# Optimization experiments

Hardware: AMD Instinct MI355X
Metric: run time of the kernel (lower is better)

The kernel has to match this reference:

```python
import jax, jax.numpy as jnp
import numpy as np
from jax import lax

B, H, W = 16, 256, 256
NUM_HIDDEN = 12
C = 3 + NUM_HIDDEN + 1  # 16 channels: rgb + hidden + alpha
HID = 64
ALPHA = 1.0
THR = 0.1

SOBEL_X = jnp.array([[-1.0, 0.0, 1.0], [-2.0, 0.0, 2.0], [-1.0, 0.0, 1.0]], jnp.float32) / 8.0
SOBEL_Y = jnp.array([[-1.0, -2.0, -1.0], [0.0, 0.0, 0.0], [1.0, 2.0, 1.0]], jnp.float32) / 8.0


def _sobel_conv(s, k):
    # s: [B,H,W] channel-summed state; k: [3,3]. SAME-padded 2D stencil.
    return lax.conv_general_dilated(
        s[..., None], k[:, :, None, None], window_strides=(1, 1), padding='SAME',
        dimension_numbers=('NHWC', 'HWIO', 'NHWC'))  # [B,H,W,1]


def _alive(x, thr):
    # 3x3 max-pool over alpha channel (index 3), SAME padding.
    a = x[..., 3:4]
    pooled = lax.reduce_window(a, -jnp.inf, lax.max, (1, 3, 3, 1), (1, 1, 1, 1), 'SAME')
    return pooled > thr  # [B,H,W,1] bool


def setup_inputs() -> dict:
    key = jax.random.key(0)
    ks = jax.random.split(key, 7)
    x = jax.random.uniform(ks[0], (B, H, W, C), dtype=jnp.float32)
    # UpdateNet params: 1x1 convs stored as dense matrices [in, out].
    w1 = jax.random.normal(ks[1], (3 * C, HID), dtype=jnp.float32) * (1.0 / np.sqrt(3 * C))
    b1 = jnp.zeros((HID,), jnp.float32)
    w2 = jax.random.normal(ks[2], (HID, HID), dtype=jnp.float32) * (1.0 / np.sqrt(HID))
    b2 = jnp.zeros((HID,), jnp.float32)
    # Original zero-inits w3; use small random values so outputs/grads are nontrivial.
    w3 = jax.random.normal(ks[3], (HID, C), dtype=jnp.float32) * 0.01
    return {'x': x, 'w1': w1, 'b1': b1, 'w2': w2, 'b2': b2, 'w3': w3}


def reference(x, w1, b1, w2, b2, w3):
    pre_life = _alive(x, THR)
    # Sobel perception: kernel[o,i] = sobel for all o,i  =>  each output channel
    # is the sobel filter applied to the channel-sum; broadcast across C channels.
    s = jnp.sum(x, axis=-1)                      # [B,H,W]
    sx = _sobel_conv(s, SOBEL_X)                 # [B,H,W,1]
    sy = _sobel_conv(s, SOBEL_Y)                 # [B,H,W,1]
    perc = jnp.concatenate(
        [x, jnp.broadcast_to(sx, x.shape), jnp.broadcast_to(sy, x.shape)], axis=-1)  # [B,H,W,3C]
    # UpdateNet: two biased 1x1 convs + ReLU, then unbiased 1x1 conv.
    h = jax.nn.relu(jnp.einsum('bhwi,io->bhwo', perc, w1) + b1)
    h = jax.nn.relu(jnp.einsum('bhwi,io->bhwo', h, w2) + b2)
    update = jnp.einsum('bhwi,io->bhwo', h, w3)  # [B,H,W,C]
    # cell_fire_rate == 1.0 -> stochastic update mask is all ones.
    x_new = x + ALPHA * update
    post_life = _alive(x_new, THR)
    life = (pre_life & post_life).astype(x_new.dtype)
    return x_new * life
```

## Files before the change

### kernel.cpp

```cpp
#include <hip/hip_runtime.h>
#include <hip/hip_bf16.h>
#include <cstdint>

#define NPIX (16 * 256 * 256)
#define THRV 0.1f

typedef __bf16 bf16x8 __attribute__((ext_vector_type(8)));
typedef float  f32x4  __attribute__((ext_vector_type(4)));

#define NSLOT 18

__global__ __launch_bounds__(64) void k_pack(const float* __restrict__ w1,
                                             const float* __restrict__ b1,
                                             const float* __restrict__ w2,
                                             const float* __restrict__ b2,
                                             const float* __restrict__ w3,
                                             float4* __restrict__ wpack) {
    const int lane = threadIdx.x;
    const int r = lane & 15, g = lane >> 4;
#pragma unroll
    for (int n = 0; n < 4; ++n) {
        const int cc = n * 16 + r;
        bf16x8 f;
#pragma unroll
        for (int j = 0; j < 8; ++j) {
            float v = 0.f;
            if (j < 4) v = w1[(g * 4 + j) * 64 + cc];
            else if (g == 0 && j == 4) { for (int t = 0; t < 16; ++t) v += w1[(16 + t) * 64 + cc]; }
            else if (g == 0 && j == 5) { for (int t = 0; t < 16; ++t) v += w1[(32 + t) * 64 + cc]; }
            else if (g == 1 && j == 4) v = b1[cc];
            f[j] = (__bf16)v;
        }
        wpack[n * 64 + lane] = *(const float4*)&f;
    }
#pragma unroll
    for (int s = 0; s < 2; ++s)
#pragma unroll
        for (int n = 0; n < 4; ++n) {
            bf16x8 f;
#pragma unroll
            for (int j = 0; j < 8; ++j) {
                const int psi = (2 * s + (j >> 2)) * 16 + g * 4 + (j & 3);
                f[j] = (__bf16)w2[psi * 64 + n * 16 + r];
            }
            wpack[(4 + s * 4 + n) * 64 + lane] = *(const float4*)&f;
        }
#pragma unroll
    for (int s = 0; s < 2; ++s) {
        bf16x8 f;
#pragma unroll
        for (int j = 0; j < 8; ++j) {
            const int psi = (2 * s + (j >> 2)) * 16 + g * 4 + (j & 3);
            f[j] = (__bf16)w3[psi * 16 + r];
        }
        wpack[(12 + s) * 64 + lane] = *(const float4*)&f;
    }
#pragma unroll
    for (int n = 0; n < 4; ++n) {
        f32x4 v;
#pragma unroll
        for (int q = 0; q < 4; ++q) v[q] = b2[n * 16 + g * 4 + q];
        wpack[(14 + n) * 64 + lane] = *(const float4*)&v;
    }
}

__global__ __launch_bounds__(256) void k_fused(const float* __restrict__ x,
                                               const float4* __restrict__ wpack,
                                               float* __restrict__ out,
                                               unsigned char* __restrict__ rpre,
                                               unsigned char* __restrict__ anewf) {
    __shared__ float sH0[256], sC[256], sH2[256], sC3[256];

    const int tid = threadIdx.x;
    const int wv = tid >> 6, lane = tid & 63;
    const int r = lane & 15, g = lane >> 4;

    const int row = (blockIdx.x & 7) * 512 + (blockIdx.x >> 3);
    const int y = row & 255;
    const size_t rbase = (size_t)row * 256;
    const int wcol = wv * 64;
    const bool ymok = (y > 0), ypok = (y < 255);

    float4 ha0 = {0,0,0,0}, ha1 = {0,0,0,0}, ha2 = {0,0,0,0}, ha3 = {0,0,0,0};
    float4 hb0 = {0,0,0,0}, hb1 = {0,0,0,0}, hb2 = {0,0,0,0}, hb3 = {0,0,0,0};
    if (ymok) {
        const float4* pm = (const float4*)(x + (rbase - 256 + tid) * 16);
        ha0 = pm[0]; ha1 = pm[1]; ha2 = pm[2]; ha3 = pm[3];
    }
    if (ypok) {
        const float4* pp = (const float4*)(x + (rbase + 256 + tid) * 16);
        hb0 = pp[0]; hb1 = pp[1]; hb2 = pp[2]; hb3 = pp[3];
    }
    float4 xf[4];
#pragma unroll
    for (int t = 0; t < 4; ++t) {
        const int col = wcol + t * 16 + r;
        xf[t] = *(const float4*)(x + (rbase + col) * 16 + g * 4);
    }

    const float s0 = ((ha0.x + ha0.y) + (ha0.z + ha0.w)) + ((ha1.x + ha1.y) + (ha1.z + ha1.w)) +
                     ((ha2.x + ha2.y) + (ha2.z + ha2.w)) + ((ha3.x + ha3.y) + (ha3.z + ha3.w));
    const float s2 = ((hb0.x + hb0.y) + (hb0.z + hb0.w)) + ((hb1.x + hb1.y) + (hb1.z + hb1.w)) +
                     ((hb2.x + hb2.y) + (hb2.z + hb2.w)) + ((hb3.x + hb3.y) + (hb3.z + hb3.w));
    sH0[tid] = s0;
    sH2[tid] = s2;

#pragma unroll
    for (int t = 0; t < 4; ++t) {
        const int col = wcol + t * 16 + r;
        float p = (xf[t].x + xf[t].y) + (xf[t].z + xf[t].w);
        p += __shfl_xor(p, 16);
        p += __shfl_xor(p, 32);
        if (g == 0) { sC[col] = p; sC3[col] = xf[t].w; }
    }
    __syncthreads();

    bf16x8 w1f[4], w2f[2][4], w3f[2];
    f32x4 b2v[4];
#pragma unroll
    for (int n = 0; n < 4; ++n) { float4 t = wpack[n * 64 + lane]; w1f[n] = *(bf16x8*)&t; }
#pragma unroll
    for (int s2i = 0; s2i < 2; ++s2i)
#pragma unroll
        for (int n = 0; n < 4; ++n) { float4 t = wpack[(4 + s2i * 4 + n) * 64 + lane]; w2f[s2i][n] = *(bf16x8*)&t; }
#pragma unroll
    for (int s2i = 0; s2i < 2; ++s2i) { float4 t = wpack[(12 + s2i) * 64 + lane]; w3f[s2i] = *(bf16x8*)&t; }
#pragma unroll
    for (int n = 0; n < 4; ++n) { float4 t = wpack[(14 + n) * 64 + lane]; b2v[n] = *(f32x4*)&t; }

#pragma unroll
    for (int t = 0; t < 4; ++t) {
        const int col = wcol + t * 16 + r;
        const size_t pix = rbase + col;
        const bool cl = (col > 0), cr = (col < 255);

        const float r0m = cl ? sH0[col - 1] : 0.f;
        const float r0c = sH0[col];
        const float r0p = cr ? sH0[col + 1] : 0.f;
        const float r1m = cl ? sC[col - 1] : 0.f;
        const float r1p = cr ? sC[col + 1] : 0.f;
        const float r2m = cl ? sH2[col - 1] : 0.f;
        const float r2c = sH2[col];
        const float r2p = cr ? sH2[col + 1] : 0.f;
        const float gx = ((r0p - r0m) + 2.f * (r1p - r1m) + (r2p - r2m)) * 0.125f;
        const float gy = ((r2m + 2.f * r2c + r2p) - (r0m + 2.f * r0c + r0p)) * 0.125f;

        if (g == 0) {
            const float c3m = cl ? sC3[col - 1] : 0.f;
            const float c3c = sC3[col];
            const float c3p = cr ? sC3[col + 1] : 0.f;
            rpre[pix] = (fmaxf(c3m, fmaxf(c3c, c3p)) > THRV) ? 1 : 0;
        }

        bf16x8 a1;
        a1[0] = (__bf16)xf[t].x; a1[1] = (__bf16)xf[t].y;
        a1[2] = (__bf16)xf[t].z; a1[3] = (__bf16)xf[t].w;
        a1[4] = (__bf16)(g == 0 ? gx : (g == 1 ? 1.f : 0.f));
        a1[5] = (__bf16)(g == 0 ? gy : 0.f);
        a1[6] = (__bf16)0.f; a1[7] = (__bf16)0.f;

        f32x4 acc1[4];
#pragma unroll
        for (int n = 0; n < 4; ++n)
            acc1[n] = __builtin_amdgcn_mfma_f32_16x16x32_bf16(
                w1f[n], a1, (f32x4){0.f, 0.f, 0.f, 0.f}, 0, 0, 0);

        bf16x8 bf2[2];
#pragma unroll
        for (int s2i = 0; s2i < 2; ++s2i)
#pragma unroll
            for (int j = 0; j < 4; ++j) {
                bf2[s2i][j]     = (__bf16)fmaxf(acc1[2 * s2i][j], 0.f);
                bf2[s2i][4 + j] = (__bf16)fmaxf(acc1[2 * s2i + 1][j], 0.f);
            }

        f32x4 acc2[4];
#pragma unroll
        for (int n = 0; n < 4; ++n) {
            acc2[n] = b2v[n];
            acc2[n] = __builtin_amdgcn_mfma_f32_16x16x32_bf16(w2f[0][n], bf2[0], acc2[n], 0, 0, 0);
            acc2[n] = __builtin_amdgcn_mfma_f32_16x16x32_bf16(w2f[1][n], bf2[1], acc2[n], 0, 0, 0);
        }

        bf16x8 bf3[2];
#pragma unroll
        for (int s2i = 0; s2i < 2; ++s2i)
#pragma unroll
            for (int j = 0; j < 4; ++j) {
                bf3[s2i][j]     = (__bf16)fmaxf(acc2[2 * s2i][j], 0.f);
                bf3[s2i][4 + j] = (__bf16)fmaxf(acc2[2 * s2i + 1][j], 0.f);
            }

        f32x4 acc3 = __builtin_amdgcn_mfma_f32_16x16x32_bf16(
            w3f[0], bf3[0], (f32x4){0.f, 0.f, 0.f, 0.f}, 0, 0, 0);
        acc3 = __builtin_amdgcn_mfma_f32_16x16x32_bf16(w3f[1], bf3[1], acc3, 0, 0, 0);

        f32x4 xn;
        xn[0] = xf[t].x + acc3[0]; xn[1] = xf[t].y + acc3[1];
        xn[2] = xf[t].z + acc3[2]; xn[3] = xf[t].w + acc3[3];
        __builtin_nontemporal_store(xn, (f32x4*)(out + pix * 16 + g * 4));
        if (g == 0) anewf[pix] = (xn[3] > THRV) ? 1 : 0;
    }
}

__global__ __launch_bounds__(256) void k_post(const unsigned char* __restrict__ rpre,
                                              const unsigned char* __restrict__ anewf,
                                              float* __restrict__ out) {
    const int q = blockIdx.x * 256 + threadIdx.x;
    const int p0 = q * 4;
    const int bi = p0 >> 16;
    const int rem = p0 & 65535;
    const int y = rem >> 8;
    const int c0 = rem & 255;
    const unsigned char* pr = rpre + ((size_t)bi << 16);
    const unsigned char* an = anewf + ((size_t)bi << 16);

    unsigned pre = 0, M = 0, l = 0, rr = 0;
#pragma unroll
    for (int dy = -1; dy <= 1; ++dy) {
        const int y2 = y + dy;
        if ((unsigned)y2 >= 256u) continue;
        const int ro = y2 * 256;
        pre |= *(const unsigned*)(pr + ro + c0);
        M   |= *(const unsigned*)(an + ro + c0);
        l   |= (c0 > 0)   ? (unsigned)an[ro + c0 - 1] : 0u;
        rr  |= (c0 < 252) ? (unsigned)an[ro + c0 + 4] : 0u;
    }
    const unsigned post = M | (M << 8) | l | (M >> 8) | (rr << 24);
    const unsigned alive = pre & post;
    if (alive != 0x01010101u) {
        const f32x4 z = (f32x4){0.f, 0.f, 0.f, 0.f};
#pragma unroll
        for (int i = 0; i < 4; ++i)
            if (!((alive >> (8 * i)) & 1u)) {
                f32x4* op = (f32x4*)(out + (size_t)(p0 + i) * 16);
                op[0] = z; op[1] = z; op[2] = z; op[3] = z;
            }
    }
}

extern "C" void kernel_launch(void* const* d_in, const int* in_sizes, int n_in,
                              void* d_out, int out_size, void* d_ws, size_t ws_size,
                              hipStream_t stream) {
    const float* x  = (const float*)d_in[0];
    const float* w1 = (const float*)d_in[1];
    const float* b1 = (const float*)d_in[2];
    const float* w2 = (const float*)d_in[3];
    const float* b2 = (const float*)d_in[4];
    const float* w3 = (const float*)d_in[5];
    float* out = (float*)d_out;

    unsigned char* rpre  = (unsigned char*)d_ws;
    unsigned char* anewf = rpre + NPIX;
    float4* wpack = (float4*)(anewf + NPIX);

    hipLaunchKernelGGL(k_pack, dim3(1), dim3(64), 0, stream, w1, b1, w2, b2, w3, wpack);
    hipLaunchKernelGGL(k_fused, dim3(NPIX / 256), dim3(256), 0, stream,
                       x, wpack, out, rpre, anewf);
    hipLaunchKernelGGL(k_post, dim3(NPIX / 1024), dim3(256), 0, stream,
                       rpre, anewf, out);
}
```

Baseline: 48.74 us.

## Process two image rows per block to share halo row loads

Each block of the fused kernel now handles two consecutive rows instead of one. The two rows share the vertical halo rows, so each block loads 4 rows of input for 2 output rows rather than 3 rows for 1, cutting redundant halo traffic. The grid is halved and each wave handles 8 column tiles rather than 4, which raises register pressure and per-thread work while reducing block count. The b2 accumulator init is also folded directly into the first MFMA call, which is cosmetic.

```diff
diff --git a/kernel.cpp b/kernel.cpp
--- a/kernel.cpp
+++ b/kernel.cpp
@@ -69,49 +69,48 @@
                                                float* __restrict__ out,
                                                unsigned char* __restrict__ rpre,
                                                unsigned char* __restrict__ anewf) {
-    __shared__ float sH0[256], sC[256], sH2[256], sC3[256];
+    __shared__ float sS[4][256];
+    __shared__ float sC3[2][256];
 
     const int tid = threadIdx.x;
     const int wv = tid >> 6, lane = tid & 63;
     const int r = lane & 15, g = lane >> 4;
 
-    const int row = (blockIdx.x & 7) * 512 + (blockIdx.x >> 3);
-    const int y = row & 255;
-    const size_t rbase = (size_t)row * 256;
-    const int wcol = wv * 64;
-    const bool ymok = (y > 0), ypok = (y < 255);
-
-    float4 ha0 = {0,0,0,0}, ha1 = {0,0,0,0}, ha2 = {0,0,0,0}, ha3 = {0,0,0,0};
-    float4 hb0 = {0,0,0,0}, hb1 = {0,0,0,0}, hb2 = {0,0,0,0}, hb3 = {0,0,0,0};
+    const int pair = (blockIdx.x & 7) * 256 + (blockIdx.x >> 3);
+    const int y0row = pair * 2;
+    const int y = y0row & 255;
+    const size_t rbase0 = (size_t)y0row * 256;
+    const bool ymok = (y > 0), ypok = (y < 254);
+
+    float hs0 = 0.f, hs1 = 0.f;
     if (ymok) {
-        const float4* pm = (const float4*)(x + (rbase - 256 + tid) * 16);
-        ha0 = pm[0]; ha1 = pm[1]; ha2 = pm[2]; ha3 = pm[3];
+        const float4* pm = (const float4*)(x + (rbase0 - 256 + tid) * 16);
+        float4 a = pm[0], b = pm[1], c = pm[2], d = pm[3];
+        hs0 = ((a.x + a.y) + (a.z + a.w)) + ((b.x + b.y) + (b.z + b.w)) +
+              ((c.x + c.y) + (c.z + c.w)) + ((d.x + d.y) + (d.z + d.w));
     }
     if (ypok) {
-        const float4* pp = (const float4*)(x + (rbase + 256 + tid) * 16);
-        hb0 = pp[0]; hb1 = pp[1]; hb2 = pp[2]; hb3 = pp[3];
-    }
-    float4 xf[4];
-#pragma unroll
-    for (int t = 0; t < 4; ++t) {
-        const int col = wcol + t * 16 + r;
-        xf[t] = *(const float4*)(x + (rbase + col) * 16 + g * 4);
-    }
-
-    const float s0 = ((ha0.x + ha0.y) + (ha0.z + ha0.w)) + ((ha1.x + ha1.y) + (ha1.z + ha1.w)) +
-                     ((ha2.x + ha2.y) + (ha2.z + ha2.w)) + ((ha3.x + ha3.y) + (ha3.z + ha3.w));
-    const float s2 = ((hb0.x + hb0.y) + (hb0.z + hb0.w)) + ((hb1.x + hb1.y) + (hb1.z + hb1.w)) +
-                     ((hb2.x + hb2.y) + (hb2.z + hb2.w)) + ((hb3.x + hb3.y) + (hb3.z + hb3.w));
-    sH0[tid] = s0;
-    sH2[tid] = s2;
-
-#pragma unroll
-    for (int t = 0; t < 4; ++t) {
-        const int col = wcol + t * 16 + r;
+        const float4* pp = (const float4*)(x + (rbase0 + 512 + tid) * 16);
+        float4 a = pp[0], b = pp[1], c = pp[2], d = pp[3];
+        hs1 = ((a.x + a.y) + (a.z + a.w)) + ((b.x + b.y) + (b.z + b.w)) +
+              ((c.x + c.y) + (c.z + c.w)) + ((d.x + d.y) + (d.z + d.w));
+    }
+    sS[0][tid] = hs0;
+    sS[3][tid] = hs1;
+
+    const int rowi = wv >> 1;
+    const int colbase = (wv & 1) * 128;
+    const size_t rb = rbase0 + (size_t)rowi * 256;
+
+    float4 xf[8];
+#pragma unroll
+    for (int t = 0; t < 8; ++t) {
+        const int col = colbase + t * 16 + r;
+        xf[t] = *(const float4*)(x + (rb + col) * 16 + g * 4);
         float p = (xf[t].x + xf[t].y) + (xf[t].z + xf[t].w);
         p += __shfl_xor(p, 16);
         p += __shfl_xor(p, 32);
-        if (g == 0) { sC[col] = p; sC3[col] = xf[t].w; }
+        if (g == 0) { sS[1 + rowi][col] = p; sC3[rowi][col] = xf[t].w; }
     }
     __syncthreads();
 
@@ -129,26 +128,26 @@
     for (int n = 0; n < 4; ++n) { float4 t = wpack[(14 + n) * 64 + lane]; b2v[n] = *(f32x4*)&t; }
 
 #pragma unroll
-    for (int t = 0; t < 4; ++t) {
-        const int col = wcol + t * 16 + r;
-        const size_t pix = rbase + col;
+    for (int t = 0; t < 8; ++t) {
+        const int col = colbase + t * 16 + r;
+        const size_t pix = rb + col;
         const bool cl = (col > 0), cr = (col < 255);
 
-        const float r0m = cl ? sH0[col - 1] : 0.f;
-        const float r0c = sH0[col];
-        const float r0p = cr ? sH0[col + 1] : 0.f;
-        const float r1m = cl ? sC[col - 1] : 0.f;
-        const float r1p = cr ? sC[col + 1] : 0.f;
-        const float r2m = cl ? sH2[col - 1] : 0.f;
-        const float r2c = sH2[col];
-        const float r2p = cr ? sH2[col + 1] : 0.f;
+        const float r0m = cl ? sS[rowi][col - 1] : 0.f;
+        const float r0c = sS[rowi][col];
+        const float r0p = cr ? sS[rowi][col + 1] : 0.f;
+        const float r1m = cl ? sS[rowi + 1][col - 1] : 0.f;
+        const float r1p = cr ? sS[rowi + 1][col + 1] : 0.f;
+        const float r2m = cl ? sS[rowi + 2][col - 1] : 0.f;
+        const float r2c = sS[rowi + 2][col];
+        const float r2p = cr ? sS[rowi + 2][col + 1] : 0.f;
         const float gx = ((r0p - r0m) + 2.f * (r1p - r1m) + (r2p - r2m)) * 0.125f;
         const float gy = ((r2m + 2.f * r2c + r2p) - (r0m + 2.f * r0c + r0p)) * 0.125f;
 
         if (g == 0) {
-            const float c3m = cl ? sC3[col - 1] : 0.f;
-            const float c3c = sC3[col];
-            const float c3p = cr ? sC3[col + 1] : 0.f;
+            const float c3m = cl ? sC3[rowi][col - 1] : 0.f;
+            const float c3c = sC3[rowi][col];
+            const float c3p = cr ? sC3[rowi][col + 1] : 0.f;
             rpre[pix] = (fmaxf(c3m, fmaxf(c3c, c3p)) > THRV) ? 1 : 0;
         }
 
@@ -177,8 +176,7 @@
         f32x4 acc2[4];
 #pragma unroll
         for (int n = 0; n < 4; ++n) {
-            acc2[n] = b2v[n];
-            acc2[n] = __builtin_amdgcn_mfma_f32_16x16x32_bf16(w2f[0][n], bf2[0], acc2[n], 0, 0, 0);
+            acc2[n] = __builtin_amdgcn_mfma_f32_16x16x32_bf16(w2f[0][n], bf2[0], b2v[n], 0, 0, 0);
             acc2[n] = __builtin_amdgcn_mfma_f32_16x16x32_bf16(w2f[1][n], bf2[1], acc2[n], 0, 0, 0);
         }
 
@@ -255,7 +253,7 @@
     float4* wpack = (float4*)(anewf + NPIX);
 
     hipLaunchKernelGGL(k_pack, dim3(1), dim3(64), 0, stream, w1, b1, w2, b2, w3, wpack);
-    hipLaunchKernelGGL(k_fused, dim3(NPIX / 256), dim3(256), 0, stream,
+    hipLaunchKernelGGL(k_fused, dim3(NPIX / 512), dim3(256), 0, stream,
                        x, wpack, out, rpre, anewf);
     hipLaunchKernelGGL(k_post, dim3(NPIX / 1024), dim3(256), 0, stream,
                        rpre, anewf, out);
```

New measurement: 48.63 us. No clear change (-0.2%).
